# Kernel optimization log

Measured on AMD Instinct MI355X. Metric: run time of the kernel, lower is better.

The kernel has to match this reference:

```python
import jax, jax.numpy as jnp
import numpy as np

B, N, D, C = 8, 128, 256, 3

def setup_inputs() -> dict:
    key = jax.random.key(0)
    k1, k2, k3, k4, k5 = jax.random.split(key, 5)
    s_v = jax.random.normal(k1, (B, N, D), dtype=jnp.float32)
    s_e = jax.random.normal(k2, (B, N, N, D), dtype=jnp.float32)
    sub_graph = jax.random.randint(k3, (B,), 0, N)
    s_e_score = jax.random.uniform(k4, (B, C, N), dtype=jnp.float32)
    # per-graph node counts in [1, N], float since used as divisor
    num_node = jax.random.randint(k5, (B,), 1, N + 1).astype(jnp.float32)
    return {"s_v": s_v, "s_e": s_e, "sub_graph": sub_graph,
            "s_e_score": s_e_score, "num_node": num_node}

def reference(s_v, s_e, sub_graph, s_e_score, num_node):
    b, n, d = s_v.shape
    score2 = s_e_score[:, :2]                                   # (B,2,N)
    lam_b = jnp.sum(score2.reshape(b, -1), axis=-1, keepdims=True) + 1e-6  # (B,1)
    zero_one_hot = jnp.ones((b, n), dtype=s_v.dtype).at[:, 0].set(0.0)
    sub_graph_mask = jax.nn.one_hot(sub_graph, n, dtype=s_v.dtype) * zero_one_hot  # (B,N)
    score = jnp.sum(score2, axis=1) + sub_graph_mask            # (B,N)
    lam = score / lam_b                                         # (B,N)
    # sum_{i,j} (s_v[i] + s_e[i,j]) * lam[i] == sum_i lam[i] * (N*s_v[i] + sum_j s_e[i,j])
    # -- identical math to the torch broadcast, without the (B,N,N,D) intermediate
    agg = n * s_v + jnp.sum(s_e, axis=2)                        # (B,N,D)
    r_G = jnp.einsum('bn,bnd->bd', lam, agg)                    # (B,D)
    r_G = r_G / (num_node[:, None] ** 2)
    return r_G[:, None, :]                                      # (B,1,D)
```

## Files before the change

kernel.cpp:

```cpp
#include <hip/hip_runtime.h>

#define BB 8
#define NN 128
#define DD 256
#define NF4 (DD / 4)

__global__ __launch_bounds__(128) void prep_kernel(
    const float* __restrict__ se_score,
    const int*   __restrict__ sub_graph,
    const float* __restrict__ num_node,
    float* __restrict__ wbuf,
    float* __restrict__ out)
{
    const int b = blockIdx.x;
    const int t = threadIdx.x;

    const float s0 = se_score[b * 3 * NN + t];
    const float s1 = se_score[b * 3 * NN + NN + t];
    const float sc = s0 + s1;

    float r = sc;
    #pragma unroll
    for (int off = 32; off > 0; off >>= 1)
        r += __shfl_down(r, off, 64);
    __shared__ float wpart[2];
    if ((t & 63) == 0) wpart[t >> 6] = r;
    __syncthreads();
    const float lam_b = wpart[0] + wpart[1] + 1e-6f;

    const float mask = (sub_graph[b] == t && t != 0) ? 1.0f : 0.0f;
    const float nn = num_node[b];

    wbuf[b * NN + t] = (sc + mask) / (lam_b * nn * nn);

    out[b * DD + t] = 0.0f;
    out[b * DD + NN + t] = 0.0f;
}

__global__ __launch_bounds__(256) void reduce_kernel(
    const float4* __restrict__ se4,
    const float4* __restrict__ sv4,
    const float*  __restrict__ wbuf,
    float* __restrict__ out)
{
    const int blk = blockIdx.x;
    const int b   = blk >> 7;
    const int n   = blk & 127;
    const int tid = threadIdx.x;
    const int v   = tid & 63;
    const int s   = tid >> 6;

    const float4* __restrict__ p = se4 + (size_t)(b * NN + n) * (NN * NF4);

    float4 a0 = make_float4(0.f, 0.f, 0.f, 0.f);
    float4 a1 = make_float4(0.f, 0.f, 0.f, 0.f);
    #pragma unroll 4
    for (int m = s; m < NN; m += 8) {
        const float4 x = p[m * NF4 + v];
        const float4 y = p[(m + 4) * NF4 + v];
        a0.x += x.x; a0.y += x.y; a0.z += x.z; a0.w += x.w;
        a1.x += y.x; a1.y += y.y; a1.z += y.z; a1.w += y.w;
    }
    float4 a;
    a.x = a0.x + a1.x; a.y = a0.y + a1.y;
    a.z = a0.z + a1.z; a.w = a0.w + a1.w;

    __shared__ float4 sm[256];
    sm[tid] = a;
    __syncthreads();

    if (tid < 64) {
        const float4 t0 = sm[tid];
        const float4 t1 = sm[tid + 64];
        const float4 t2 = sm[tid + 128];
        const float4 t3 = sm[tid + 192];
        const float  w  = wbuf[b * NN + n];
        const float4 sv = sv4[(size_t)(b * NN + n) * NF4 + v];

        const float rx = w * (128.0f * sv.x + t0.x + t1.x + t2.x + t3.x);
        const float ry = w * (128.0f * sv.y + t0.y + t1.y + t2.y + t3.y);
        const float rz = w * (128.0f * sv.z + t0.z + t1.z + t2.z + t3.z);
        const float rw = w * (128.0f * sv.w + t0.w + t1.w + t2.w + t3.w);

        float* o = out + b * DD + v * 4;
        atomicAdd(o + 0, rx);
        atomicAdd(o + 1, ry);
        atomicAdd(o + 2, rz);
        atomicAdd(o + 3, rw);
    }
}

extern "C" void kernel_launch(void* const* d_in, const int* in_sizes, int n_in,
                              void* d_out, int out_size, void* d_ws, size_t ws_size,
                              hipStream_t stream) {
    const float* s_v       = (const float*)d_in[0];
    const float* s_e       = (const float*)d_in[1];
    const int*   sub_graph = (const int*)  d_in[2];
    const float* s_e_score = (const float*)d_in[3];
    const float* num_node  = (const float*)d_in[4];
    float* out  = (float*)d_out;
    float* wbuf = (float*)d_ws;

    prep_kernel<<<BB, NN, 0, stream>>>(s_e_score, sub_graph, num_node, wbuf, out);
    reduce_kernel<<<BB * NN, 256, 0, stream>>>(
        (const float4*)s_e, (const float4*)s_v, wbuf, out);
}
```

Baseline: 205.8 us.

## Fuse weight prep into main reduction and replace atomics with two-pass reduce

The separate prep kernel is removed. Each reduction block now computes its lambda normaliser and per-node weight inline from the score inputs. Instead of atomically adding per-node contributions into the output, each block writes its weighted partial row to workspace. A second small kernel then sums the 128 partials per batch. This is meant to remove atomic contention and the need to zero the output, at the cost of an extra workspace write and read of about 1 MB and one more tiny launch.

```diff
diff --git a/kernel.cpp b/kernel.cpp
--- a/kernel.cpp
+++ b/kernel.cpp
@@ -5,43 +5,13 @@
 #define DD 256
 #define NF4 (DD / 4)
 
-__global__ __launch_bounds__(128) void prep_kernel(
-    const float* __restrict__ se_score,
-    const int*   __restrict__ sub_graph,
-    const float* __restrict__ num_node,
-    float* __restrict__ wbuf,
-    float* __restrict__ out)
-{
-    const int b = blockIdx.x;
-    const int t = threadIdx.x;
-
-    const float s0 = se_score[b * 3 * NN + t];
-    const float s1 = se_score[b * 3 * NN + NN + t];
-    const float sc = s0 + s1;
-
-    float r = sc;
-    #pragma unroll
-    for (int off = 32; off > 0; off >>= 1)
-        r += __shfl_down(r, off, 64);
-    __shared__ float wpart[2];
-    if ((t & 63) == 0) wpart[t >> 6] = r;
-    __syncthreads();
-    const float lam_b = wpart[0] + wpart[1] + 1e-6f;
-
-    const float mask = (sub_graph[b] == t && t != 0) ? 1.0f : 0.0f;
-    const float nn = num_node[b];
-
-    wbuf[b * NN + t] = (sc + mask) / (lam_b * nn * nn);
-
-    out[b * DD + t] = 0.0f;
-    out[b * DD + NN + t] = 0.0f;
-}
-
-__global__ __launch_bounds__(256) void reduce_kernel(
+__global__ __launch_bounds__(256) void pass1_kernel(
     const float4* __restrict__ se4,
     const float4* __restrict__ sv4,
-    const float*  __restrict__ wbuf,
-    float* __restrict__ out)
+    const float*  __restrict__ se_score,
+    const int*    __restrict__ sub_graph,
+    const float*  __restrict__ num_node,
+    float4* __restrict__ ws4)
 {
     const int blk = blockIdx.x;
     const int b   = blk >> 7;
@@ -49,6 +19,17 @@
     const int tid = threadIdx.x;
     const int v   = tid & 63;
     const int s   = tid >> 6;
+
+    __shared__ float red[4];
+    {
+        float x = se_score[b * 3 * NN + tid];
+        #pragma unroll
+        for (int off = 32; off > 0; off >>= 1)
+            x += __shfl_down(x, off, 64);
+        if ((tid & 63) == 0) red[tid >> 6] = x;
+    }
+    __syncthreads();
+    const float lam_b = red[0] + red[1] + red[2] + red[3] + 1e-6f;
 
     const float4* __restrict__ p = se4 + (size_t)(b * NN + n) * (NN * NF4);
 
@@ -74,19 +55,57 @@
         const float4 t1 = sm[tid + 64];
         const float4 t2 = sm[tid + 128];
         const float4 t3 = sm[tid + 192];
-        const float  w  = wbuf[b * NN + n];
+
+        const float sc   = se_score[b * 3 * NN + n] + se_score[b * 3 * NN + NN + n];
+        const float mask = (sub_graph[b] == n && n != 0) ? 1.0f : 0.0f;
+        const float nnum = num_node[b];
+        const float w    = (sc + mask) / (lam_b * nnum * nnum);
+
         const float4 sv = sv4[(size_t)(b * NN + n) * NF4 + v];
 
-        const float rx = w * (128.0f * sv.x + t0.x + t1.x + t2.x + t3.x);
-        const float ry = w * (128.0f * sv.y + t0.y + t1.y + t2.y + t3.y);
-        const float rz = w * (128.0f * sv.z + t0.z + t1.z + t2.z + t3.z);
-        const float rw = w * (128.0f * sv.w + t0.w + t1.w + t2.w + t3.w);
+        float4 r;
+        r.x = w * (128.0f * sv.x + t0.x + t1.x + t2.x + t3.x);
+        r.y = w * (128.0f * sv.y + t0.y + t1.y + t2.y + t3.y);
+        r.z = w * (128.0f * sv.z + t0.z + t1.z + t2.z + t3.z);
+        r.w = w * (128.0f * sv.w + t0.w + t1.w + t2.w + t3.w);
 
-        float* o = out + b * DD + v * 4;
-        atomicAdd(o + 0, rx);
-        atomicAdd(o + 1, ry);
-        atomicAdd(o + 2, rz);
-        atomicAdd(o + 3, rw);
+        ws4[(size_t)(b * NN + n) * NF4 + v] = r;
+    }
+}
+
+__global__ __launch_bounds__(256) void pass2_kernel(
+    const float4* __restrict__ ws4,
+    float4* __restrict__ out4)
+{
+    const int b    = blockIdx.x;
+    const int tid  = threadIdx.x;
+    const int v    = tid & 63;
+    const int part = tid >> 6;
+
+    const float4* __restrict__ p = ws4 + (size_t)b * NN * NF4;
+
+    float4 a = make_float4(0.f, 0.f, 0.f, 0.f);
+    #pragma unroll 8
+    for (int n = part * 32; n < part * 32 + 32; ++n) {
+        const float4 x = p[n * NF4 + v];
+        a.x += x.x; a.y += x.y; a.z += x.z; a.w += x.w;
+    }
+
+    __shared__ float4 sm[256];
+    sm[tid] = a;
+    __syncthreads();
+
+    if (tid < 64) {
+        const float4 t0 = sm[tid];
+        const float4 t1 = sm[tid + 64];
+        const float4 t2 = sm[tid + 128];
+        const float4 t3 = sm[tid + 192];
+        float4 r;
+        r.x = t0.x + t1.x + t2.x + t3.x;
+        r.y = t0.y + t1.y + t2.y + t3.y;
+        r.z = t0.z + t1.z + t2.z + t3.z;
+        r.w = t0.w + t1.w + t2.w + t3.w;
+        out4[b * NF4 + v] = r;
     }
 }
 
@@ -98,10 +117,10 @@
     const int*   sub_graph = (const int*)  d_in[2];
     const float* s_e_score = (const float*)d_in[3];
     const float* num_node  = (const float*)d_in[4];
-    float* out  = (float*)d_out;
-    float* wbuf = (float*)d_ws;
+    float4* out4 = (float4*)d_out;
+    float4* ws4  = (float4*)d_ws;
 
-    prep_kernel<<<BB, NN, 0, stream>>>(s_e_score, sub_graph, num_node, wbuf, out);
-    reduce_kernel<<<BB * NN, 256, 0, stream>>>(
-        (const float4*)s_e, (const float4*)s_v, wbuf, out);
+    pass1_kernel<<<BB * NN, 256, 0, stream>>>(
+        (const float4*)s_e, (const float4*)s_v, s_e_score, sub_graph, num_node, ws4);
+    pass2_kernel<<<BB, 256, 0, stream>>>(ws4, out4);
 }
```

New measurement: 200.7 us. 1.03x faster.
